# Performance work log

Measured on AMD Instinct MI355X. Metric: run time of the kernel, lower is better.

Reference implementation:

```python
import jax, jax.numpy as jnp
import numpy as np

TAU = 1.0
EPS = 1e-5


def _gcn_sparse(x, src, dst, ew, W, b, n):
    # PyG GCNConv: add self-loops (weight 1), sym-normalize, aggregate src->dst
    deg = jax.ops.segment_sum(ew, dst, num_segments=n) + 1.0
    dinv = jnp.where(deg > 0, jax.lax.rsqrt(deg), 0.0)
    h = x @ W
    coef = dinv[src] * ew * dinv[dst]              # [E]
    out = jax.ops.segment_sum(h[src] * coef[:, None], dst, num_segments=n)
    out = out + h * (dinv * dinv)[:, None]         # self-loop term
    return out + b


def _gcn_dense(x, A, W, b):
    # x: [B,N,d], A: [B,N,N] with A[b,i,j] = weight of edge j->i
    n = A.shape[-1]
    Ah = A + jnp.eye(n, dtype=A.dtype)
    deg = Ah.sum(-1)
    dinv = jnp.where(deg > 0, jax.lax.rsqrt(deg), 0.0)
    An = dinv[:, :, None] * Ah * dinv[:, None, :]
    return jnp.einsum('bij,bjd->bid', An, x @ W) + b


def _bn_silu(x, g, be, axes):
    # BatchNorm over node axis (training-mode batch stats, biased var) + SiLU
    m = x.mean(axes, keepdims=True)
    v = x.var(axes, keepdims=True)
    return jax.nn.silu(g * (x - m) * jax.lax.rsqrt(v + EPS) + be)


def setup_inputs() -> dict:
    key = jax.random.key(0)
    ks = jax.random.split(key, 12)
    B, NPG, EPER = 32, 1024, 16384
    CIN, C, K1, K2, OUT = 64, 128, 128, 32, 10
    N, E = B * NPG, B * EPER
    ei = jax.random.randint(ks[0], (2, E), 0, NPG, dtype=jnp.int32)
    off = jnp.repeat(jnp.arange(B, dtype=jnp.int32) * NPG, EPER)
    edge_index = ei + off[None, :]
    x = jax.random.normal(ks[1], (N, CIN), jnp.float32)
    batch = jnp.repeat(jnp.arange(B, dtype=jnp.int32), NPG)
    batch_ptr = jnp.arange(B + 1, dtype=jnp.int32) * NPG
    p = lambda k, s: jax.random.normal(k, s, jnp.float32) * 0.05
    return dict(
        x=x, edge_index=edge_index, batch=batch, batch_ptr=batch_ptr,
        w1a=p(ks[2], (CIN, C)), b1a=jnp.zeros((C,)), g1a=jnp.ones((C,)), be1a=jnp.zeros((C,)),
        w1b=p(ks[3], (C, C)), b1b=jnp.zeros((C,)), g1b=jnp.ones((C,)), be1b=jnp.zeros((C,)),
        wp1=p(ks[4], (C, K1)), bp1=jnp.zeros((K1,)),
        w2a=p(ks[5], (C, C)), b2a=jnp.zeros((C,)), g2a=jnp.ones((C,)), be2a=jnp.zeros((C,)),
        w2b=p(ks[6], (C, C)), b2b=jnp.zeros((C,)), g2b=jnp.ones((C,)), be2b=jnp.zeros((C,)),
        wp2=p(ks[7], (C, K2)), bp2=jnp.zeros((K2,)),
        wl=p(ks[8], (C, OUT)), bl=jnp.zeros((OUT,)))


def reference(x, edge_index, batch, batch_ptr,
              w1a, b1a, g1a, be1a, w1b, b1b, g1b, be1b, wp1, bp1,
              w2a, b2a, g2a, be2a, w2b, b2b, g2b, be2b, wp2, bp2,
              wl, bl):
    n = x.shape[0]
    B = batch_ptr.shape[0] - 1
    npg = n // B                                    # uniform nodes per graph
    src, dst = edge_index[0], edge_index[1]
    ew = jnp.ones((edge_index.shape[1],), x.dtype)  # edge_weight=None -> ones

    # ---- stack 1: sparse GCN residual blocks + stochastic pool ----
    h = _bn_silu(_gcn_sparse(x, src, dst, ew, w1a, b1a, n), g1a, be1a, 0)
    h = h + _bn_silu(_gcn_sparse(h, src, dst, ew, w1b, b1b, n), g1b, be1b, 0)
    s = jax.nn.softmax(_gcn_sparse(h, src, dst, ew, wp1, bp1, n) / TAU, -1)  # [n,K1]
    s3 = s.reshape(B, npg, -1)
    x2 = jnp.einsum('bnc,bnd->bcd', s3, h.reshape(B, npg, -1))   # s^T x  [B,K1,C]
    t = jax.ops.segment_sum(s[src] * ew[:, None], dst, num_segments=n)  # A s
    A2 = jnp.einsum('bnc,bnk->bck', s3, t.reshape(B, npg, -1))   # s^T A s [B,K1,K1]

    # ---- stack 2: dense GCN on pooled graph + stochastic pool ----
    h2 = _bn_silu(_gcn_dense(x2, A2, w2a, b2a), g2a, be2a, (0, 1))
    h2 = h2 + _bn_silu(_gcn_dense(h2, A2, w2b, b2b), g2b, be2b, (0, 1))
    s2 = jax.nn.softmax(_gcn_dense(h2, A2, wp2, bp2) / TAU, -1)  # [B,K1,K2]
    x3 = jnp.einsum('bnc,bnd->bcd', s2, h2)                      # [B,K2,C]

    # global mean pool over nodes per graph, linear, log_softmax
    g = x3.mean(axis=1)
    out = jax.nn.log_softmax(g @ wl + bl, axis=1)
    # aux losses are multiplied by 0 in the original forward -> exact zero
    return (out, jnp.zeros((), x.dtype))
```

## Files before the change

### kernel.cpp

```cpp
#include <hip/hip_runtime.h>
#include <cmath>

#define KSPLIT 8
#define ELL_ST 80

typedef __attribute__((ext_vector_type(8))) short short8;
typedef __attribute__((ext_vector_type(4))) float float4v;

static __device__ __forceinline__ unsigned short f2bf(float f){
  union { float f; unsigned u; } c; c.f = f;
  unsigned r = c.u + 0x7fff + ((c.u >> 16) & 1);
  return (unsigned short)(r >> 16);
}
static __device__ __forceinline__ float u2f(unsigned u){
  union { unsigned u; float f; } c; c.u = u; return c.f;
}
static __device__ __forceinline__ float silu(float y){ return y/(1.f+__expf(-y)); }

static __device__ __forceinline__ void coef_prologue(const float* __restrict__ stats,
                                                     const float* __restrict__ gamma,
                                                     const float* __restrict__ beta,
                                                     float invM, float* lds, int tbase){
  int t = threadIdx.x - tbase;
  if(t >= 0 && t < 128){
    float s = 0.f, q = 0.f;
    #pragma unroll
    for(int k=0;k<8;k++){ s += stats[k*128+t]; q += stats[1024 + k*128+t]; }
    float m = s*invM;
    float v = q*invM - m*m;
    float sc = gamma[t]*rsqrtf(v + 1e-5f);
    lds[t] = sc;
    lds[128+t] = beta[t] - m*sc;
  }
}

__global__ void k_fill_ell(const int* __restrict__ src, const int* __restrict__ dst,
                           int* __restrict__ cursor, int* __restrict__ esrc, int E){
  int e = blockIdx.x*256 + threadIdx.x;
  if(e<E){
    int d = dst[e];
    int p = atomicAdd(&cursor[d], 1);
    if(p < ELL_ST) esrc[(size_t)d*ELL_ST + p] = src[e];
  }
}

__global__ void k_dinv_wt(const int* __restrict__ deg, float* __restrict__ dinv, int n,
                          const float* __restrict__ w1a, const float* __restrict__ w1b,
                          const float* __restrict__ wp1, unsigned short* __restrict__ t1a,
                          unsigned short* __restrict__ t1b, unsigned short* __restrict__ tp1,
                          int CIN){
  int i = blockIdx.x*256 + threadIdx.x;
  if(i < n){ dinv[i] = rsqrtf((float)deg[i] + 1.0f); }
  int j = i - n;
  int n1 = CIN*128, n2 = 128*128;
  if(j >= 0 && j < n1){
    int k = j >> 7, c = j & 127;
    t1a[(size_t)c*CIN + k] = f2bf(w1a[j]);
  } else if(j >= n1 && j < n1+n2){
    int jj = j - n1; int k = jj >> 7, c = jj & 127;
    t1b[(size_t)c*128 + k] = f2bf(w1b[jj]);
  } else if(j >= n1+n2 && j < n1+2*n2){
    int jj = j - n1 - n2; int k = jj >> 7, c = jj & 127;
    tp1[(size_t)c*128 + k] = f2bf(wp1[jj]);
  }
}

__global__ void k_gemm_mfma(const float* __restrict__ A, const float* __restrict__ A2,
                            const unsigned short* __restrict__ Bt,
                            unsigned short* __restrict__ Cb, int M, int K, int Nc,
                            const float* __restrict__ rowscale,
                            const float* __restrict__ stA, const float* __restrict__ gA,
                            const float* __restrict__ beA,
                            const float* __restrict__ stB, const float* __restrict__ gB,
                            const float* __restrict__ beB, float invM){
  __shared__ unsigned short Abf[64][40];
  __shared__ unsigned short Bbf[64][40];
  __shared__ float lcA[256], lcB[256];
  int tid = threadIdx.x;
  if(stA) coef_prologue(stA, gA, beA, invM, lcA, 0);
  if(stB) coef_prologue(stB, gB, beB, invM, lcB, 128);
  if(stA || stB) __syncthreads();
  int wv = tid >> 6, lane = tid & 63;
  int quad = lane >> 4, l16 = lane & 15;
  int row0 = blockIdx.y*64, col0 = blockIdx.x*64;
  int sr = tid >> 2, sk = (tid & 3)*8;
  float4v acc[4] = {};
  for(int kt=0; kt<K; kt+=32){
    const float* ap = &A[(size_t)(row0+sr)*K + kt + sk];
    float va[8];
    *(float4*)&va[0] = *(const float4*)ap;
    *(float4*)&va[4] = *(const float4*)(ap+4);
    if(stB){
      const float* bp = &A2[(size_t)(row0+sr)*K + kt + sk];
      float vb[8];
      *(float4*)&vb[0] = *(const float4*)bp;
      *(float4*)&vb[4] = *(const float4*)(bp+4);
      #pragma unroll
      for(int i=0;i<8;i++){
        int c = kt+sk+i;
        va[i] = silu(lcA[c]*va[i] + lcA[128+c]) + silu(lcB[c]*vb[i] + lcB[128+c]);
      }
    } else if(stA){
      #pragma unroll
      for(int i=0;i<8;i++){
        int c = kt+sk+i;
        va[i] = silu(lcA[c]*va[i] + lcA[128+c]);
      }
    }
    uint4 pk;
    pk.x = (unsigned)f2bf(va[0]) | ((unsigned)f2bf(va[1])<<16);
    pk.y = (unsigned)f2bf(va[2]) | ((unsigned)f2bf(va[3])<<16);
    pk.z = (unsigned)f2bf(va[4]) | ((unsigned)f2bf(va[5])<<16);
    pk.w = (unsigned)f2bf(va[6]) | ((unsigned)f2bf(va[7])<<16);
    *(uint4*)&Abf[sr][sk] = pk;
    *(uint4*)&Bbf[sr][sk] = *(const uint4*)&Bt[(size_t)(col0+sr)*K + kt + sk];
    __syncthreads();
    short8 af = *(const short8*)&Abf[wv*16 + l16][quad*8];
    #pragma unroll
    for(int t=0;t<4;t++){
      short8 bf = *(const short8*)&Bbf[t*16 + l16][quad*8];
      acc[t] = __builtin_amdgcn_mfma_f32_16x16x32_bf16(af, bf, acc[t], 0, 0, 0);
    }
    __syncthreads();
  }
  float scr[4];
  #pragma unroll
  for(int r=0;r<4;r++){
    int grow = row0 + wv*16 + quad*4 + r;
    scr[r] = rowscale ? rowscale[grow] : 1.f;
  }
  #pragma unroll
  for(int t=0;t<4;t++){
    #pragma unroll
    for(int r=0;r<4;r++){
      int grow = row0 + wv*16 + quad*4 + r;
      int gcol = col0 + t*16 + l16;
      Cb[(size_t)grow*Nc + gcol] = f2bf(acc[t][r]*scr[r]);
    }
  }
}

__global__ void k_gemm64(const float* __restrict__ A, const float* __restrict__ B,
                         float* __restrict__ C, int M, int K, int Nc,
                         const float* __restrict__ rowscale,
                         const float* __restrict__ stA, const float* __restrict__ gA,
                         const float* __restrict__ beA, float invM){
  __shared__ float As[16][68];
  __shared__ float Bs[16][68];
  __shared__ float lc[256];
  int tid = threadIdx.x;
  if(stA){ coef_prologue(stA, gA, beA, invM, lc, 0); __syncthreads(); }
  int tx = tid & 15, ty = tid >> 4;
  int row0 = blockIdx.y*64, col0 = blockIdx.x*64;
  float acc[4][4] = {};
  for(int kt=0; kt<K; kt+=16){
    int ra = tid >> 2, ka = (tid & 3)*4;
    float4 va = *(const float4*)&A[(size_t)(row0+ra)*K + kt + ka];
    if(stA){
      float vv[4] = {va.x, va.y, va.z, va.w};
      #pragma unroll
      for(int i=0;i<4;i++){
        int c = kt+ka+i;
        vv[i] = silu(lc[c]*vv[i] + lc[128+c]);
      }
      va.x=vv[0]; va.y=vv[1]; va.z=vv[2]; va.w=vv[3];
    }
    As[ka+0][ra]=va.x; As[ka+1][ra]=va.y; As[ka+2][ra]=va.z; As[ka+3][ra]=va.w;
    int rb = tid >> 4, cb = (tid & 15)*4;
    *(float4*)&Bs[rb][cb] = *(const float4*)&B[(size_t)(kt+rb)*Nc + col0 + cb];
    __syncthreads();
    #pragma unroll
    for(int k=0;k<16;k++){
      float4 a = *(const float4*)&As[k][ty*4];
      float4 b = *(const float4*)&Bs[k][tx*4];
      float av[4]={a.x,a.y,a.z,a.w}, bv[4]={b.x,b.y,b.z,b.w};
      #pragma unroll
      for(int i=0;i<4;i++)
        #pragma unroll
        for(int j=0;j<4;j++) acc[i][j] += av[i]*bv[j];
    }
    __syncthreads();
  }
  #pragma unroll
  for(int i=0;i<4;i++){
    int r = row0 + ty*4 + i;
    float sc = rowscale ? rowscale[r] : 1.0f;
    float4 v; v.x=acc[i][0]*sc; v.y=acc[i][1]*sc; v.z=acc[i][2]*sc; v.w=acc[i][3]*sc;
    *(float4*)&C[(size_t)r*Nc + col0 + tx*4] = v;
  }
}

template<bool DO_SOFTMAX, bool GCN, bool STATS, bool BF16IN, bool BF16OUT>
__global__ void k_gather(const int* __restrict__ degc, const int* __restrict__ esrc,
                         const float* __restrict__ dinv, const void* __restrict__ hWs,
                         const float* __restrict__ bias, float* __restrict__ out,
                         float* __restrict__ stats){
  __shared__ float lsum[4][128];
  __shared__ float lsq[4][128];
  const unsigned short* h16 = (const unsigned short*)hWs;
  const float* h32 = (const float*)hWs;
  int wave = threadIdx.x >> 6;
  int lane = threadIdx.x & 63;
  int bid = blockIdx.x;
  int d = ((bid & 7) << 12) | ((bid >> 3) << 2) | wave;
  int grp = lane >> 5;
  int c4 = (lane & 31)*4;
  int cnt = degc[d]; if(cnt > ELL_ST) cnt = ELL_ST;
  cnt = __builtin_amdgcn_readfirstlane(cnt);
  const int* row = esrc + (size_t)d*ELL_ST;

  auto loadrow = [&](int s)->float4{
    if(BF16IN){
      uint2 u = *(const uint2*)&h16[(size_t)s*128 + c4];
      float4 v;
      v.x = u2f(u.x << 16); v.y = u2f(u.x & 0xffff0000u);
      v.z = u2f(u.y << 16); v.w = u2f(u.y & 0xffff0000u);
      return v;
    } else {
      return *(const float4*)&h32[(size_t)s*128 + c4];
    }
  };

  float4 a0 = {0.f,0.f,0.f,0.f}, a1 = {0.f,0.f,0.f,0.f};
  float4 a2 = {0.f,0.f,0.f,0.f}, a3 = {0.f,0.f,0.f,0.f};
  if(GCN && grp == 0)
    a0 = loadrow(d);
  for(int base=0; base<cnt; base+=32){
    int m = cnt - base; if(m > 32) m = 32;
    int idx = (lane < m) ? row[base + lane] : 0;
    int full = m & ~7;
    int j0 = 0;
    for(; j0 < full; j0 += 8){
      int s0 = __shfl(idx, j0+grp);
      int s1 = __shfl(idx, j0+grp+2);
      int s2 = __shfl(idx, j0+grp+4);
      int s3 = __shfl(idx, j0+grp+6);
      float4 v0 = loadrow(s0);
      float4 v1 = loadrow(s1);
      float4 v2 = loadrow(s2);
      float4 v3 = loadrow(s3);
      a0.x+=v0.x; a0.y+=v0.y; a0.z+=v0.z; a0.w+=v0.w;
      a1.x+=v1.x; a1.y+=v1.y; a1.z+=v1.z; a1.w+=v1.w;
      a2.x+=v2.x; a2.y+=v2.y; a2.z+=v2.z; a2.w+=v2.w;
      a3.x+=v3.x; a3.y+=v3.y; a3.z+=v3.z; a3.w+=v3.w;
    }
    if(j0 < m){
      int jj0 = j0+grp, jj1 = j0+grp+2, jj2 = j0+grp+4, jj3 = j0+grp+6;
      int s0 = __shfl(idx, jj0 < m ? jj0 : 0);
      int s1 = __shfl(idx, jj1 < m ? jj1 : 0);
      int s2 = __shfl(idx, jj2 < m ? jj2 : 0);
      int s3 = __shfl(idx, jj3 < m ? jj3 : 0);
      if(jj0 < m){ float4 v = loadrow(s0);
        a0.x+=v.x; a0.y+=v.y; a0.z+=v.z; a0.w+=v.w; }
      if(jj1 < m){ float4 v = loadrow(s1);
        a1.x+=v.x; a1.y+=v.y; a1.z+=v.z; a1.w+=v.w; }
      if(jj2 < m){ float4 v = loadrow(s2);
        a2.x+=v.x; a2.y+=v.y; a2.z+=v.z; a2.w+=v.w; }
      if(jj3 < m){ float4 v = loadrow(s3);
        a3.x+=v.x; a3.y+=v.y; a3.z+=v.z; a3.w+=v.w; }
    }
  }
  float4 acc;
  acc.x = (a0.x+a1.x)+(a2.x+a3.x);
  acc.y = (a0.y+a1.y)+(a2.y+a3.y);
  acc.z = (a0.z+a1.z)+(a2.z+a3.z);
  acc.w = (a0.w+a1.w)+(a2.w+a3.w);
  acc.x += __shfl_xor(acc.x, 32);
  acc.y += __shfl_xor(acc.y, 32);
  acc.z += __shfl_xor(acc.z, 32);
  acc.w += __shfl_xor(acc.w, 32);
  float4 val = acc;
  if(GCN){
    float dv = dinv[d];
    float4 bi = *(const float4*)&bias[c4];
    val.x = dv*acc.x + bi.x; val.y = dv*acc.y + bi.y;
    val.z = dv*acc.z + bi.z; val.w = dv*acc.w + bi.w;
  }
  if(DO_SOFTMAX){
    float mx = fmaxf(fmaxf(val.x,val.y), fmaxf(val.z,val.w));
    #pragma unroll
    for(int o=1;o<32;o<<=1) mx = fmaxf(mx, __shfl_xor(mx,o));
    float4 e; e.x=__expf(val.x-mx); e.y=__expf(val.y-mx);
    e.z=__expf(val.z-mx); e.w=__expf(val.w-mx);
    float s = e.x+e.y+e.z+e.w;
    #pragma unroll
    for(int o=1;o<32;o<<=1) s += __shfl_xor(s,o);
    float inv = 1.f/s;
    val.x=e.x*inv; val.y=e.y*inv; val.z=e.z*inv; val.w=e.w*inv;
  }
  if(grp == 0){
    if(BF16OUT){
      unsigned short* o16 = (unsigned short*)out;
      uint2 w;
      w.x = (unsigned)f2bf(val.x) | ((unsigned)f2bf(val.y)<<16);
      w.y = (unsigned)f2bf(val.z) | ((unsigned)f2bf(val.w)<<16);
      *(uint2*)&o16[(size_t)d*128 + c4] = w;
    } else {
      *(float4*)&out[(size_t)d*128 + c4] = val;
    }
  }
  if(STATS){
    if(grp == 0){
      *(float4*)&lsum[wave][c4] = val;
      float4 q; q.x=val.x*val.x; q.y=val.y*val.y; q.z=val.z*val.z; q.w=val.w*val.w;
      *(float4*)&lsq[wave][c4] = q;
    }
    __syncthreads();
    int t = threadIdx.x;
    if(t < 128){
      float s = (lsum[0][t]+lsum[1][t]) + (lsum[2][t]+lsum[3][t]);
      atomicAdd(&stats[(bid & 7)*128 + t], s);
    } else {
      int c = t - 128;
      float q = (lsq[0][c]+lsq[1][c]) + (lsq[2][c]+lsq[3][c]);
      atomicAdd(&stats[1024 + (bid & 7)*128 + c], q);
    }
  }
}

__global__ __launch_bounds__(256, 2)
void k_pool2(const unsigned short* __restrict__ P, const float* __restrict__ Qa,
             const float* __restrict__ Qb, const unsigned short* __restrict__ Qc,
             const float* __restrict__ stA, const float* __restrict__ gA,
             const float* __restrict__ beA,
             const float* __restrict__ stB, const float* __restrict__ gB,
             const float* __restrict__ beB, float invM,
             float* __restrict__ part1, float* __restrict__ part2, int npg, int nb){
  __shared__ float Ps[2][8][132], Qs[2][8][132];
  __shared__ float lcA[256], lcB[256];
  int tid = threadIdx.x;
  bool fused = (blockIdx.z == 0);
  if(fused){
    coef_prologue(stA, gA, beA, invM, lcA, 0);
    coef_prologue(stB, gB, beB, invM, lcB, 128);
    __syncthreads();
  }
  int ks = blockIdx.x, b = blockIdx.y;
  int klen = npg / KSPLIT;
  size_t base = ((size_t)b*npg + (size_t)ks*klen)*128;
  int tx = tid & 15, ty = tid >> 4;
  int r = tid >> 5, c4s = (tid & 31)*4;
  size_t off = (size_t)r*128 + c4s;

  auto ldbf = [&](const unsigned short* p, size_t idx)->float4{
    uint2 u = *(const uint2*)&p[idx];
    float4 v;
    v.x = u2f(u.x << 16); v.y = u2f(u.x & 0xffff0000u);
    v.z = u2f(u.y << 16); v.w = u2f(u.y & 0xffff0000u);
    return v;
  };
  auto stage_q = [&](float4 qa, float4 qb)->float4{
    float4 q;
    q.x = silu(lcA[c4s+0]*qa.x+lcA[128+c4s+0]) + silu(lcB[c4s+0]*qb.x+lcB[128+c4s+0]);
    q.y = silu(lcA[c4s+1]*qa.y+lcA[128+c4s+1]) + silu(lcB[c4s+1]*qb.y+lcB[128+c4s+1]);
    q.z = silu(lcA[c4s+2]*qa.z+lcA[128+c4s+2]) + silu(lcB[c4s+2]*qb.z+lcB[128+c4s+2]);
    q.w = silu(lcA[c4s+3]*qa.w+lcA[128+c4s+3]) + silu(lcB[c4s+3]*qb.w+lcB[128+c4s+3]);
    return q;
  };

  {
    float4 p0 = ldbf(P, base + off);
    float4 q0;
    if(fused){
      float4 qa0 = *(const float4*)&Qa[base + off];
      float4 qb0 = *(const float4*)&Qb[base + off];
      q0 = stage_q(qa0, qb0);
    } else {
      q0 = ldbf(Qc, base + off);
    }
    *(float4*)&Ps[0][r][c4s] = p0;
    *(float4*)&Qs[0][r][c4s] = q0;
  }
  __syncthreads();

  float acc[8][8] = {};
  int chunks = klen >> 3;
  for(int c=0; c<chunks; c++){
    float4 pn, qan, qbn, qn;
    if(c+1 < chunks){
      size_t nb2 = base + (size_t)((c+1)*8)*128 + off;
      pn = ldbf(P, nb2);
      if(fused){
        qan = *(const float4*)&Qa[nb2];
        qbn = *(const float4*)&Qb[nb2];
      } else {
        qn = ldbf(Qc, nb2);
      }
    }
    int cb = c & 1;
    #pragma unroll
    for(int k=0;k<8;k++){
      float4 a0 = *(const float4*)&Ps[cb][k][ty*4];
      float4 a1 = *(const float4*)&Ps[cb][k][64+ty*4];
      float4 b0 = *(const float4*)&Qs[cb][k][tx*4];
      float4 b1 = *(const float4*)&Qs[cb][k][64+tx*4];
      float av[8]={a0.x,a0.y,a0.z,a0.w,a1.x,a1.y,a1.z,a1.w};
      float bv[8]={b0.x,b0.y,b0.z,b0.w,b1.x,b1.y,b1.z,b1.w};
      #pragma unroll
      for(int i=0;i<8;i++)
        #pragma unroll
        for(int j=0;j<8;j++) acc[i][j] += av[i]*bv[j];
    }
    if(c+1 < chunks){
      int nbuf = (c+1) & 1;
      *(float4*)&Ps[nbuf][r][c4s] = pn;
      *(float4*)&Qs[nbuf][r][c4s] = fused ? stage_q(qan, qbn) : qn;
    }
    __syncthreads();
  }

  float* outp = (fused ? part1 : part2) + ((size_t)(ks*nb + b)*128)*128;
  #pragma unroll
  for(int ih=0; ih<2; ih++)
    #pragma unroll
    for(int ii=0; ii<4; ii++){
      int i = ih*64 + ty*4 + ii;
      #pragma unroll
      for(int jh=0; jh<2; jh++){
        float4 v;
        v.x = acc[ih*4+ii][jh*4+0];
        v.y = acc[ih*4+ii][jh*4+1];
        v.z = acc[ih*4+ii][jh*4+2];
        v.w = acc[ih*4+ii][jh*4+3];
        *(float4*)&outp[(size_t)i*128 + jh*64 + tx*4] = v;
      }
    }
}

__global__ void k_pool_reduce2(const float* __restrict__ p1, const float* __restrict__ p2,
                               float* __restrict__ x2, float* __restrict__ A2,
                               float* __restrict__ dinv2, int total){
  int i = blockIdx.x*256 + threadIdx.x;
  int half = total >> 2;
  if(i < half){
    float4 s = *(const float4*)&p1[(size_t)i*4];
    #pragma unroll
    for(int ks=1; ks<KSPLIT; ks++){
      float4 v = *(const float4*)&p1[(size_t)ks*total + (size_t)i*4];
      s.x+=v.x; s.y+=v.y; s.z+=v.z; s.w+=v.w;
    }
    *(float4*)&x2[(size_t)i*4] = s;
  } else {
    int ia = i - half;
    float4 s = *(const float4*)&p2[(size_t)ia*4];
    #pragma unroll
    for(int ks=1; ks<KSPLIT; ks++){
      float4 v = *(const float4*)&p2[(size_t)ks*total + (size_t)ia*4];
      s.x+=v.x; s.y+=v.y; s.z+=v.z; s.w+=v.w;
    }
    *(float4*)&A2[(size_t)ia*4] = s;
    float rs = s.x+s.y+s.z+s.w;
    #pragma unroll
    for(int o=16;o>0;o>>=1) rs += __shfl_xor(rs, o);
    if((threadIdx.x & 31) == 0) dinv2[ia>>5] = rsqrtf(rs + 1.0f);
  }
}

__global__ void k_bgemm_post_stats(const float* __restrict__ A, const float* __restrict__ X,
                                   const float* __restrict__ dinv2, const float* __restrict__ bias,
                                   float* __restrict__ outp, float* __restrict__ stats){
  __shared__ float As[16][17], Xs[16][17];
  __shared__ float rs[16][17], rq[16][17];
  int b = blockIdx.z;
  int i0 = blockIdx.y*16, j0 = blockIdx.x*16;
  int tx = threadIdx.x, ty = threadIdx.y;
  const float* Ab = A + (size_t)b*16384;
  const float* Xb = X + (size_t)b*16384;
  float acc = 0.f;
  for(int k0=0;k0<128;k0+=16){
    As[ty][tx] = Ab[(i0+ty)*128 + k0+tx];
    Xs[ty][tx] = Xb[(k0+ty)*128 + j0+tx];
    __syncthreads();
    #pragma unroll
    for(int k=0;k<16;k++) acc += As[ty][k]*Xs[k][tx];
    __syncthreads();
  }
  int gr = b*128 + i0 + ty;
  float v = dinv2[gr]*(acc + Xb[(i0+ty)*128 + j0+tx]) + bias[j0+tx];
  outp[(size_t)gr*128 + j0+tx] = v;
  rs[ty][tx] = v; rq[ty][tx] = v*v;
  __syncthreads();
  if(ty == 0){
    float s = 0.f, q = 0.f;
    #pragma unroll
    for(int k=0;k<16;k++){ s += rs[k][tx]; q += rq[k][tx]; }
    int slot = b & 7;
    atomicAdd(&stats[slot*128 + j0+tx], s);
    atomicAdd(&stats[1024 + slot*128 + j0+tx], q);
  }
}

__global__ void k_final(const float* __restrict__ dTa, const float* __restrict__ dTb,
                        const float* __restrict__ stA, const float* __restrict__ gA,
                        const float* __restrict__ beA,
                        const float* __restrict__ stB, const float* __restrict__ gB,
                        const float* __restrict__ beB, float invMc,
                        const float* __restrict__ wl, const float* __restrict__ bl,
                        float* __restrict__ out, int K1n, int Cc, float inv_k2,
                        int OUTc, int zero_idx){
  __shared__ float lcA[256], lcB[256];
  __shared__ float red[256];
  __shared__ float gsh[128];
  __shared__ float logits[32];
  __shared__ float mred, lred;
  coef_prologue(stA, gA, beA, invMc, lcA, 0);
  coef_prologue(stB, gB, beB, invMc, lcB, 128);
  __syncthreads();
  int b = blockIdx.x;
  int tid = threadIdx.x;
  int c = tid & 127, rh = tid >> 7;
  const float* pa = dTa + (size_t)b*K1n*Cc;
  const float* pb = dTb + (size_t)b*K1n*Cc;
  float sa = lcA[c], ha = lcA[128+c], sb = lcB[c], hb = lcB[128+c];
  float acc = 0.f;
  for(int r = rh; r < K1n; r += 2){
    float ya = sa*pa[(size_t)r*Cc + c] + ha;
    float yb = sb*pb[(size_t)r*Cc + c] + hb;
    acc += silu(ya) + silu(yb);
  }
  red[tid] = acc;
  __syncthreads();
  if(tid < 128) gsh[tid] = (red[tid] + red[tid+128]) * inv_k2;
  __syncthreads();
  if(tid < OUTc){
    float l = bl[tid];
    for(int d=0; d<Cc; d++) l += gsh[d]*wl[d*OUTc + tid];
    logits[tid] = l;
  }
  __syncthreads();
  if(tid==0){
    float m = -1e30f;
    for(int o=0;o<OUTc;o++) m = fmaxf(m, logits[o]);
    float s = 0.f;
    for(int o=0;o<OUTc;o++) s += __expf(logits[o]-m);
    mred = m; lred = logf(s);
  }
  __syncthreads();
  if(tid < OUTc) out[b*OUTc + tid] = logits[tid] - mred - lred;
  if(b==0 && tid==0 && zero_idx >= 0) out[zero_idx] = 0.f;
}

extern "C" void kernel_launch(void* const* d_in, const int* in_sizes, int n_in,
                              void* d_out, int out_size, void* d_ws, size_t ws_size,
                              hipStream_t stream){
  const float* x    = (const float*)d_in[0];
  const int*   ei   = (const int*)d_in[1];
  const float* w1a  = (const float*)d_in[4];
  const float* b1a  = (const float*)d_in[5];
  const float* g1a  = (const float*)d_in[6];
  const float* be1a = (const float*)d_in[7];
  const float* w1b  = (const float*)d_in[8];
  const float* b1b  = (const float*)d_in[9];
  const float* g1b  = (const float*)d_in[10];
  const float* be1b = (const float*)d_in[11];
  const float* wp1  = (const float*)d_in[12];
  const float* bp1  = (const float*)d_in[13];
  const float* w2a  = (const float*)d_in[14];
  const float* b2a  = (const float*)d_in[15];
  const float* g2a  = (const float*)d_in[16];
  const float* be2a = (const float*)d_in[17];
  const float* w2b  = (const float*)d_in[18];
  const float* b2b  = (const float*)d_in[19];
  const float* g2b  = (const float*)d_in[20];
  const float* be2b = (const float*)d_in[21];
  const float* wl   = (const float*)d_in[24];
  const float* bl   = (const float*)d_in[25];
  float* out = (float*)d_out;

  const int C_   = in_sizes[5];
  const int CIN_ = in_sizes[4]/C_;
  const int N    = in_sizes[0]/CIN_;
  const int E    = in_sizes[1]/2;
  const int B_   = in_sizes[3]-1;
  const int NPG_ = N/B_;
  const int K1_  = in_sizes[13];
  const int K2_  = in_sizes[23];
  const int OUTc = in_sizes[25];
  const int M2   = B_*K1_;
  const int total = M2*C_;

  const int* srcI = ei;
  const int* dstI = ei + E;

  float* ws = (float*)d_ws;
  size_t o = 0;
  float* dinv  = ws + o; o += (size_t)N;
  unsigned short* bufW = (unsigned short*)(ws + o); o += (size_t)N*C_/2;
  float* bufA  = ws + o; o += (size_t)N*C_;
  float* bufB  = ws + o; o += (size_t)N*C_;
  unsigned short* bufS = (unsigned short*)(ws + o); o += (size_t)N*C_/2;
  unsigned short* bufT = (unsigned short*)(ws + o); o += (size_t)N*C_/2;
  float* x2    = ws + o; o += (size_t)total;
  float* A2    = ws + o; o += (size_t)total;
  float* dinv2 = ws + o; o += (size_t)M2;
  float* st1a  = ws + o; o += 2048;
  float* st1b  = ws + o; o += 2048;
  float* stDa  = ws + o; o += 2048;
  float* stDb  = ws + o; o += 2048;
  int* cursor  = (int*)(ws + o); o += (size_t)N;
  float* part  = ws + o; o += (size_t)KSPLIT*total;
  float* part2 = ws + o; o += (size_t)KSPLIT*total;
  float* dW  = part;
  float* dTa = part + (size_t)total;
  float* dTb = part + 2*(size_t)total;
  unsigned short* wt1a = (unsigned short*)(ws + o); o += (size_t)CIN_*C_/2 + 64;
  unsigned short* wt1b = (unsigned short*)(ws + o); o += (size_t)C_*C_/2 + 64;
  unsigned short* wtp1 = (unsigned short*)(ws + o); o += (size_t)C_*C_/2 + 64;
  int* esrc    = (int*)(ws + o); o += (size_t)N*ELL_ST;
  (void)ws_size; (void)n_in;

  dim3 blk256(256);
  dim3 gblk(16,16);
  auto g1 = [](int n){ return dim3((unsigned)((n+255)/256)); };
  const float invN = 1.0f/N, invM2 = 1.0f/M2;

  hipMemsetAsync(st1a, 0, (size_t)4*2048*sizeof(float) + (size_t)N*sizeof(int), stream);
  k_fill_ell<<<g1(E), blk256, 0, stream>>>(srcI, dstI, cursor, esrc, E);
  k_dinv_wt<<<g1(N + CIN_*C_ + 2*C_*C_), blk256, 0, stream>>>(cursor, dinv, N,
      w1a, w1b, wp1, wt1a, wt1b, wtp1, CIN_);

  dim3 gath((unsigned)(N/4));

  k_gemm_mfma<<<dim3(C_/64, N/64), blk256, 0, stream>>>(x, nullptr, wt1a, bufW, N, CIN_, C_, dinv,
      nullptr, nullptr, nullptr, nullptr, nullptr, nullptr, 0.f);
  k_gather<false,true,true,true,false><<<gath, blk256, 0, stream>>>(cursor, esrc, dinv, bufW, b1a, bufA, st1a);

  k_gemm_mfma<<<dim3(C_/64, N/64), blk256, 0, stream>>>(bufA, nullptr, wt1b, bufW, N, C_, C_, dinv,
      st1a, g1a, be1a, nullptr, nullptr, nullptr, invN);
  k_gather<false,true,true,true,false><<<gath, blk256, 0, stream>>>(cursor, esrc, dinv, bufW, b1b, bufB, st1b);

  k_gemm_mfma<<<dim3(K1_/64, N/64), blk256, 0, stream>>>(bufA, bufB, wtp1, bufW, N, C_, K1_, dinv,
      st1a, g1a, be1a, st1b, g1b, be1b, invN);
  k_gather<true,true,false,true,true><<<gath, blk256, 0, stream>>>(cursor, esrc, dinv, bufW, bp1, (float*)bufS, nullptr);
  k_gather<false,false,false,true,true><<<gath, blk256, 0, stream>>>(cursor, esrc, nullptr, bufS, nullptr, (float*)bufT, nullptr);

  k_pool2<<<dim3(KSPLIT, B_, 2), blk256, 0, stream>>>(bufS, bufA, bufB, bufT,
      st1a, g1a, be1a, st1b, g1b, be1b, invN, part, part2, NPG_, B_);
  k_pool_reduce2<<<g1(total/2), blk256, 0, stream>>>(part, part2, x2, A2, dinv2, total);

  k_gemm64<<<dim3(C_/64, M2/64), blk256, 0, stream>>>(x2, w2a, dW, M2, C_, C_, dinv2,
      nullptr, nullptr, nullptr, 0.f);
  k_bgemm_post_stats<<<dim3(C_/16, K1_/16, B_), gblk, 0, stream>>>(A2, dW, dinv2, b2a, dTa, stDa);

  k_gemm64<<<dim3(C_/64, M2/64), blk256, 0, stream>>>(dTa, w2b, dW, M2, C_, C_, dinv2,
      stDa, g2a, be2a, invM2);
  k_bgemm_post_stats<<<dim3(C_/16, K1_/16, B_), gblk, 0, stream>>>(A2, dW, dinv2, b2b, dTb, stDb);

  int zero_idx = (out_size > B_*OUTc) ? B_*OUTc : -1;
  k_final<<<dim3((unsigned)B_), blk256, 0, stream>>>(dTa, dTb,
      stDa, g2a, be2a, stDb, g2b, be2b, invM2, wl, bl, out, K1_, C_, 1.0f/K2_,
      OUTc, zero_idx);
}
```

Before: 382.5 us.

## Use MFMA for pooling GEMM and fuse ELL fill with weight transpose

The pooling kernel's s^T x and s^T t products move from an FP32 register-tiled outer product to bf16 MFMA. Operands are transposed into LDS, so the fused BN+SiLU result is now rounded to bf16. The ELL build and weight-transpose kernels are merged into one launch. The dinv array is dropped and rsqrt(deg+1) is recomputed from the degree counts inside the GEMM epilogue and the gather. This trades a launch and a buffer for some extra rsqrt work, and adds precision loss in the pooling GEMM.

```diff
diff --git a/kernel.cpp b/kernel.cpp
--- a/kernel.cpp
+++ b/kernel.cpp
@@ -34,41 +34,37 @@
   }
 }
 
-__global__ void k_fill_ell(const int* __restrict__ src, const int* __restrict__ dst,
-                           int* __restrict__ cursor, int* __restrict__ esrc, int E){
-  int e = blockIdx.x*256 + threadIdx.x;
-  if(e<E){
-    int d = dst[e];
-    int p = atomicAdd(&cursor[d], 1);
-    if(p < ELL_ST) esrc[(size_t)d*ELL_ST + p] = src[e];
-  }
-}
-
-__global__ void k_dinv_wt(const int* __restrict__ deg, float* __restrict__ dinv, int n,
+__global__ void k_fill_wt(const int* __restrict__ src, const int* __restrict__ dst,
+                          int* __restrict__ cursor, int* __restrict__ esrc, int E,
                           const float* __restrict__ w1a, const float* __restrict__ w1b,
                           const float* __restrict__ wp1, unsigned short* __restrict__ t1a,
                           unsigned short* __restrict__ t1b, unsigned short* __restrict__ tp1,
                           int CIN){
   int i = blockIdx.x*256 + threadIdx.x;
-  if(i < n){ dinv[i] = rsqrtf((float)deg[i] + 1.0f); }
-  int j = i - n;
-  int n1 = CIN*128, n2 = 128*128;
-  if(j >= 0 && j < n1){
-    int k = j >> 7, c = j & 127;
-    t1a[(size_t)c*CIN + k] = f2bf(w1a[j]);
-  } else if(j >= n1 && j < n1+n2){
-    int jj = j - n1; int k = jj >> 7, c = jj & 127;
-    t1b[(size_t)c*128 + k] = f2bf(w1b[jj]);
-  } else if(j >= n1+n2 && j < n1+2*n2){
-    int jj = j - n1 - n2; int k = jj >> 7, c = jj & 127;
-    tp1[(size_t)c*128 + k] = f2bf(wp1[jj]);
+  if(i < E){
+    int d = dst[i];
+    int p = atomicAdd(&cursor[d], 1);
+    if(p < ELL_ST) esrc[(size_t)d*ELL_ST + p] = src[i];
+  } else {
+    int j = i - E;
+    int n1 = CIN*128, n2 = 128*128;
+    if(j >= 0 && j < n1){
+      int k = j >> 7, c = j & 127;
+      t1a[(size_t)c*CIN + k] = f2bf(w1a[j]);
+    } else if(j >= n1 && j < n1+n2){
+      int jj = j - n1; int k = jj >> 7, c = jj & 127;
+      t1b[(size_t)c*128 + k] = f2bf(w1b[jj]);
+    } else if(j >= n1+n2 && j < n1+2*n2){
+      int jj = j - n1 - n2; int k = jj >> 7, c = jj & 127;
+      tp1[(size_t)c*128 + k] = f2bf(wp1[jj]);
+    }
   }
 }
 
 __global__ void k_gemm_mfma(const float* __restrict__ A, const float* __restrict__ A2,
                             const unsigned short* __restrict__ Bt,
                             unsigned short* __restrict__ Cb, int M, int K, int Nc,
-                            const float* __restrict__ rowscale,
+                            const int* __restrict__ rowdeg,
                             const float* __restrict__ stA, const float* __restrict__ gA,
                             const float* __restrict__ beA,
                             const float* __restrict__ stB, const float* __restrict__ gB,
@@ -127,7 +123,7 @@
   #pragma unroll
   for(int r=0;r<4;r++){
     int grow = row0 + wv*16 + quad*4 + r;
-    scr[r] = rowscale ? rowscale[grow] : 1.f;
+    scr[r] = rowdeg ? rsqrtf((float)rowdeg[grow] + 1.0f) : 1.f;
   }
   #pragma unroll
   for(int t=0;t<4;t++){
@@ -192,7 +188,7 @@
 
 template<bool DO_SOFTMAX, bool GCN, bool STATS, bool BF16IN, bool BF16OUT>
 __global__ void k_gather(const int* __restrict__ degc, const int* __restrict__ esrc,
-                         const float* __restrict__ dinv, const void* __restrict__ hWs,
+                         const void* __restrict__ hWs,
                          const float* __restrict__ bias, float* __restrict__ out,
                          float* __restrict__ stats){
   __shared__ float lsum[4][128];
@@ -205,7 +201,8 @@
   int d = ((bid & 7) << 12) | ((bid >> 3) << 2) | wave;
   int grp = lane >> 5;
   int c4 = (lane & 31)*4;
-  int cnt = degc[d]; if(cnt > ELL_ST) cnt = ELL_ST;
+  int dgr = degc[d];
+  int cnt = dgr > ELL_ST ? ELL_ST : dgr;
   cnt = __builtin_amdgcn_readfirstlane(cnt);
   const int* row = esrc + (size_t)d*ELL_ST;
 
@@ -271,7 +268,7 @@
   acc.w += __shfl_xor(acc.w, 32);
   float4 val = acc;
   if(GCN){
-    float dv = dinv[d];
+    float dv = rsqrtf((float)dgr + 1.0f);
     float4 bi = *(const float4*)&bias[c4];
     val.x = dv*acc.x + bi.x; val.y = dv*acc.y + bi.y;
     val.z = dv*acc.z + bi.z; val.w = dv*acc.w + bi.w;
@@ -326,7 +323,8 @@
              const float* __restrict__ stB, const float* __restrict__ gB,
              const float* __restrict__ beB, float invM,
              float* __restrict__ part1, float* __restrict__ part2, int npg, int nb){
-  __shared__ float Ps[2][8][132], Qs[2][8][132];
+  __shared__ unsigned short sT[128][40];
+  __shared__ unsigned short qT[128][40];
   __shared__ float lcA[256], lcB[256];
   int tid = threadIdx.x;
   bool fused = (blockIdx.z == 0);
@@ -338,92 +336,87 @@
   int ks = blockIdx.x, b = blockIdx.y;
   int klen = npg / KSPLIT;
   size_t base = ((size_t)b*npg + (size_t)ks*klen)*128;
-  int tx = tid & 15, ty = tid >> 4;
-  int r = tid >> 5, c4s = (tid & 31)*4;
-  size_t off = (size_t)r*128 + c4s;
-
-  auto ldbf = [&](const unsigned short* p, size_t idx)->float4{
-    uint2 u = *(const uint2*)&p[idx];
-    float4 v;
-    v.x = u2f(u.x << 16); v.y = u2f(u.x & 0xffff0000u);
-    v.z = u2f(u.y << 16); v.w = u2f(u.y & 0xffff0000u);
-    return v;
-  };
-  auto stage_q = [&](float4 qa, float4 qb)->float4{
-    float4 q;
-    q.x = silu(lcA[c4s+0]*qa.x+lcA[128+c4s+0]) + silu(lcB[c4s+0]*qb.x+lcB[128+c4s+0]);
-    q.y = silu(lcA[c4s+1]*qa.y+lcA[128+c4s+1]) + silu(lcB[c4s+1]*qb.y+lcB[128+c4s+1]);
-    q.z = silu(lcA[c4s+2]*qa.z+lcA[128+c4s+2]) + silu(lcB[c4s+2]*qb.z+lcB[128+c4s+2]);
-    q.w = silu(lcA[c4s+3]*qa.w+lcA[128+c4s+3]) + silu(lcB[c4s+3]*qb.w+lcB[128+c4s+3]);
-    return q;
-  };
-
-  {
-    float4 p0 = ldbf(P, base + off);
-    float4 q0;
-    if(fused){
-      float4 qa0 = *(const float4*)&Qa[base + off];
-      float4 qb0 = *(const float4*)&Qb[base + off];
-      q0 = stage_q(qa0, qb0);
+  int wv = tid >> 6, lane = tid & 63;
+  int quad = lane >> 4, l16 = lane & 15;
+  int wr = (wv >> 1)*64, wc = (wv & 1)*64;
+  int arr = tid >> 7;
+  int t7 = tid & 127;
+  int sg = (t7 >> 4)*16;
+  int sr2 = (t7 & 15)*2;
+  float4v acc[4][4] = {};
+
+  for(int c0 = 0; c0 < klen; c0 += 32){
+    size_t i0 = base + (size_t)(c0+sr2)*128 + sg;
+    if(arr == 0){
+      uint4 ua = *(const uint4*)&P[i0];
+      uint4 ub = *(const uint4*)&P[i0+8];
+      uint4 uc = *(const uint4*)&P[i0+128];
+      uint4 ud = *(const uint4*)&P[i0+136];
+      unsigned short lo[16], hi[16];
+      *(uint4*)&lo[0]=ua; *(uint4*)&lo[8]=ub;
+      *(uint4*)&hi[0]=uc; *(uint4*)&hi[8]=ud;
+      #pragma unroll
+      for(int j=0;j<16;j++)
+        *(unsigned*)&sT[sg+j][sr2] = (unsigned)lo[j] | ((unsigned)hi[j]<<16);
+    } else if(fused){
+      float va[16], vb[16], wa[16], wb[16];
+      *(float4*)&va[0]  = *(const float4*)&Qa[i0];
+      *(float4*)&va[4]  = *(const float4*)&Qa[i0+4];
+      *(float4*)&va[8]  = *(const float4*)&Qa[i0+8];
+      *(float4*)&va[12] = *(const float4*)&Qa[i0+12];
+      *(float4*)&wa[0]  = *(const float4*)&Qa[i0+128];
+      *(float4*)&wa[4]  = *(const float4*)&Qa[i0+132];
+      *(float4*)&wa[8]  = *(const float4*)&Qa[i0+136];
+      *(float4*)&wa[12] = *(const float4*)&Qa[i0+140];
+      *(float4*)&vb[0]  = *(const float4*)&Qb[i0];
+      *(float4*)&vb[4]  = *(const float4*)&Qb[i0+4];
+      *(float4*)&vb[8]  = *(const float4*)&Qb[i0+8];
+      *(float4*)&vb[12] = *(const float4*)&Qb[i0+12];
+      *(float4*)&wb[0]  = *(const float4*)&Qb[i0+128];
+      *(float4*)&wb[4]  = *(const float4*)&Qb[i0+132];
+      *(float4*)&wb[8]  = *(const float4*)&Qb[i0+136];
+      *(float4*)&wb[12] = *(const float4*)&Qb[i0+140];
+      #pragma unroll
+      for(int j=0;j<16;j++){
+        int c = sg + j;
+        float lo = silu(lcA[c]*va[j]+lcA[128+c]) + silu(lcB[c]*vb[j]+lcB[128+c]);
+        float hi = silu(lcA[c]*wa[j]+lcA[128+c]) + silu(lcB[c]*wb[j]+lcB[128+c]);
+        *(unsigned*)&qT[c][sr2] = (unsigned)f2bf(lo) | ((unsigned)f2bf(hi)<<16);
+      }
     } else {
-      q0 = ldbf(Qc, base + off);
-    }
-    *(float4*)&Ps[0][r][c4s] = p0;
-    *(float4*)&Qs[0][r][c4s] = q0;
-  }
-  __syncthreads();
-
-  float acc[8][8] = {};
-  int chunks = klen >> 3;
-  for(int c=0; c<chunks; c++){
-    float4 pn, qan, qbn, qn;
-    if(c+1 < chunks){
-      size_t nb2 = base + (size_t)((c+1)*8)*128 + off;
-      pn = ldbf(P, nb2);
-      if(fused){
-        qan = *(const float4*)&Qa[nb2];
-        qbn = *(const float4*)&Qb[nb2];
-      } else {
-        qn = ldbf(Qc, nb2);
+      uint4 ua = *(const uint4*)&Qc[i0];
+      uint4 ub = *(const uint4*)&Qc[i0+8];
+      uint4 uc = *(const uint4*)&Qc[i0+128];
+      uint4 ud = *(const uint4*)&Qc[i0+136];
+      unsigned short lo[16], hi[16];
+      *(uint4*)&lo[0]=ua; *(uint4*)&lo[8]=ub;
+      *(uint4*)&hi[0]=uc; *(uint4*)&hi[8]=ud;
+      #pragma unroll
+      for(int j=0;j<16;j++)
+        *(unsigned*)&qT[sg+j][sr2] = (unsigned)lo[j] | ((unsigned)hi[j]<<16);
+    }
+    __syncthreads();
+    #pragma unroll
+    for(int i=0;i<4;i++){
+      short8 af = *(const short8*)&sT[wr + i*16 + l16][quad*8];
+      #pragma unroll
+      for(int j=0;j<4;j++){
+        short8 bf = *(const short8*)&qT[wc + j*16 + l16][quad*8];
+        acc[i][j] = __builtin_amdgcn_mfma_f32_16x16x32_bf16(af, bf, acc[i][j], 0, 0, 0);
       }
-    }
-    int cb = c & 1;
-    #pragma unroll
-    for(int k=0;k<8;k++){
-      float4 a0 = *(const float4*)&Ps[cb][k][ty*4];
-      float4 a1 = *(const float4*)&Ps[cb][k][64+ty*4];
-      float4 b0 = *(const float4*)&Qs[cb][k][tx*4];
-      float4 b1 = *(const float4*)&Qs[cb][k][64+tx*4];
-      float av[8]={a0.x,a0.y,a0.z,a0.w,a1.x,a1.y,a1.z,a1.w};
-      float bv[8]={b0.x,b0.y,b0.z,b0.w,b1.x,b1.y,b1.z,b1.w};
-      #pragma unroll
-      for(int i=0;i<8;i++)
-        #pragma unroll
-        for(int j=0;j<8;j++) acc[i][j] += av[i]*bv[j];
-    }
-    if(c+1 < chunks){
-      int nbuf = (c+1) & 1;
-      *(float4*)&Ps[nbuf][r][c4s] = pn;
-      *(float4*)&Qs[nbuf][r][c4s] = fused ? stage_q(qan, qbn) : qn;
     }
     __syncthreads();
   }
 
   float* outp = (fused ? part1 : part2) + ((size_t)(ks*nb + b)*128)*128;
   #pragma unroll
-  for(int ih=0; ih<2; ih++)
-    #pragma unroll
-    for(int ii=0; ii<4; ii++){
-      int i = ih*64 + ty*4 + ii;
-      #pragma unroll
-      for(int jh=0; jh<2; jh++){
-        float4 v;
-        v.x = acc[ih*4+ii][jh*4+0];
-        v.y = acc[ih*4+ii][jh*4+1];
-        v.z = acc[ih*4+ii][jh*4+2];
-        v.w = acc[ih*4+ii][jh*4+3];
-        *(float4*)&outp[(size_t)i*128 + jh*64 + tx*4] = v;
-      }
+  for(int i=0;i<4;i++)
+    #pragma unroll
+    for(int r=0;r<4;r++){
+      int m = wr + i*16 + quad*4 + r;
+      #pragma unroll
+      for(int j=0;j<4;j++)
+        outp[(size_t)m*128 + wc + j*16 + l16] = acc[i][j][r];
     }
 }
 
@@ -584,7 +577,6 @@
 
   float* ws = (float*)d_ws;
   size_t o = 0;
-  float* dinv  = ws + o; o += (size_t)N;
   unsigned short* bufW = (unsigned short*)(ws + o); o += (size_t)N*C_/2;
   float* bufA  = ws + o; o += (size_t)N*C_;
   float* bufB  = ws + o; o += (size_t)N*C_;
@@ -615,24 +607,23 @@
   const float invN = 1.0f/N, invM2 = 1.0f/M2;
 
   hipMemsetAsync(st1a, 0, (size_t)4*2048*sizeof(float) + (size_t)N*sizeof(int), stream);
-  k_fill_ell<<<g1(E), blk256, 0, stream>>>(srcI, dstI, cursor, esrc, E);
-  k_dinv_wt<<<g1(N + CIN_*C_ + 2*C_*C_), blk256, 0, stream>>>(cursor, dinv, N,
+  k_fill_wt<<<g1(E + CIN_*C_ + 2*C_*C_), blk256, 0, stream>>>(srcI, dstI, cursor, esrc, E,
       w1a, w1b, wp1, wt1a, wt1b, wtp1, CIN_);
 
   dim3 gath((unsigned)(N/4));
 
-  k_gemm_mfma<<<dim3(C_/64, N/64), blk256, 0, stream>>>(x, nullptr, wt1a, bufW, N, CIN_, C_, dinv,
+  k_gemm_mfma<<<dim3(C_/64, N/64), blk256, 0, stream>>>(x, nullptr, wt1a, bufW, N, CIN_, C_, cursor,
       nullptr, nullptr, nullptr, nullptr, nullptr, nullptr, 0.f);
-  k_gather<false,true,true,true,false><<<gath, blk256, 0, stream>>>(cursor, esrc, dinv, bufW, b1a, bufA, st1a);
-
-  k_gemm_mfma<<<dim3(C_/64, N/64), blk256, 0, stream>>>(bufA, nullptr, wt1b, bufW, N, C_, C_, dinv,
+  k_gather<false,true,true,true,false><<<gath, blk256, 0, stream>>>(cursor, esrc, bufW, b1a, bufA, st1a);
+
+  k_gemm_mfma<<<dim3(C_/64, N/64), blk256, 0, stream>>>(bufA, nullptr, wt1b, bufW, N, C_, C_, cursor,
       st1a, g1a, be1a, nullptr, nullptr, nullptr, invN);
-  k_gather<false,true,true,true,false><<<gath, blk256, 0, stream>>>(cursor, esrc, dinv, bufW, b1b, bufB, st1b);
-
-  k_gemm_mfma<<<dim3(K1_/64, N/64), blk256, 0, stream>>>(bufA, bufB, wtp1, bufW, N, C_, K1_, dinv,
+  k_gather<false,true,true,true,false><<<gath, blk256, 0, stream>>>(cursor, esrc, bufW, b1b, bufB, st1b);
+
+  k_gemm_mfma<<<dim3(K1_/64, N/64), blk256, 0, stream>>>(bufA, bufB, wtp1, bufW, N, C_, K1_, cursor,
       st1a, g1a, be1a, st1b, g1b, be1b, invN);
-  k_gather<true,true,false,true,true><<<gath, blk256, 0, stream>>>(cursor, esrc, dinv, bufW, bp1, (float*)bufS, nullptr);
-  k_gather<false,false,false,true,true><<<gath, blk256, 0, stream>>>(cursor, esrc, nullptr, bufS, nullptr, (float*)bufT, nullptr);
+  k_gather<true,true,false,true,true><<<gath, blk256, 0, stream>>>(cursor, esrc, bufW, bp1, (float*)bufS, nullptr);
+  k_gather<false,false,false,true,true><<<gath, blk256, 0, stream>>>(cursor, esrc, bufS, nullptr, (float*)bufT, nullptr);
 
   k_pool2<<<dim3(KSPLIT, B_, 2), blk256, 0, stream>>>(bufS, bufA, bufB, bufT,
       st1a, g1a, be1a, st1b, g1b, be1b, invN, part, part2, NPG_, B_);
```

New measurement: 370.0 us. 1.03x faster.
